# Performance work log

Hardware: AMD Instinct MI355X
Metric: run time of the kernel (lower is better)

The kernel has to match this reference:

```python
import jax, jax.numpy as jnp
import numpy as np

N = 20000          # num proposals (nodes)
E = 320000         # num edges
IN = 4096          # roi feature dim
EMB = 200          # glove embed dim
HID = 512          # hidden dim
NH = 8             # heads (conv1)
HC = HID // NH     # 64 per-head channels
NCLS = 151         # VG object classes
NEG_SLOPE = 0.2    # PyG GATConv leaky_relu slope


def setup_inputs() -> dict:
    key = jax.random.key(0)
    ks = jax.random.split(key, 18)
    d_in1 = IN + EMB + 128  # 4424, conv1 input dim
    inp = {
        "roi_features": jax.random.normal(ks[0], (N, IN), jnp.float32),
        "box_info": jax.random.uniform(ks[1], (N, 9), jnp.float32),
        # embedding tables
        "emb1": jax.random.normal(ks[2], (NCLS, EMB), jnp.float32) * 0.02,
        "emb2": jax.random.normal(ks[3], (NCLS, EMB), jnp.float32) * 0.02,
        # bbox MLP 9 -> 32 -> 128
        "bw1": jax.random.normal(ks[4], (9, 32), jnp.float32) / np.sqrt(9),
        "bb1": jnp.zeros((32,), jnp.float32),
        "bw2": jax.random.normal(ks[5], (32, 128), jnp.float32) / np.sqrt(32),
        "bb2": jnp.zeros((128,), jnp.float32),
        # GATConv1: d_in1 -> 8 heads x 64, concat
        "W1": jax.random.normal(ks[6], (d_in1, NH * HC), jnp.float32) / np.sqrt(d_in1),
        "a_src1": jax.random.normal(ks[7], (NH, HC), jnp.float32) * 0.1,
        "a_dst1": jax.random.normal(ks[8], (NH, HC), jnp.float32) * 0.1,
        "bias1": jnp.zeros((NH * HC,), jnp.float32),
        # GATConv2: 512 -> 512, 1 head, concat=False
        "W2": jax.random.normal(ks[9], (HID, HID), jnp.float32) / np.sqrt(HID),
        "a_src2": jax.random.normal(ks[10], (1, HID), jnp.float32) * 0.1,
        "a_dst2": jax.random.normal(ks[11], (1, HID), jnp.float32) * 0.1,
        "bias2": jnp.zeros((HID,), jnp.float32),
        # int inputs
        "obj_labels": jax.random.randint(ks[12], (N,), 0, NCLS, jnp.int32),
        "edge_index": jax.random.randint(ks[13], (2, E), 0, N, jnp.int32),
    }
    return inp


def _segment_softmax(logits, seg, n):
    # logits: [E, H]; softmax over edges sharing the same destination seg id
    m = jax.ops.segment_max(logits, seg, num_segments=n)
    e = jnp.exp(logits - m[seg])
    s = jax.ops.segment_sum(e, seg, num_segments=n)
    return e / (s[seg] + 1e-16)


def _gat_conv(x, src, dst, W, a_src, a_dst, bias, concat):
    # PyG GATConv (self-loops already included in src/dst); dropout off (eval)
    n = x.shape[0]
    H, C = a_src.shape
    h = (x @ W).reshape(n, H, C)                      # [N, H, C]
    al_s = jnp.einsum('nhc,hc->nh', h, a_src)         # [N, H]
    al_d = jnp.einsum('nhc,hc->nh', h, a_dst)
    logits = jax.nn.leaky_relu(al_s[src] + al_d[dst], NEG_SLOPE)  # [E, H]
    alpha = _segment_softmax(logits, dst, n)          # [E, H]
    out = jax.ops.segment_sum(alpha[:, :, None] * h[src], dst, num_segments=n)
    out = out.reshape(n, H * C) if concat else out.mean(axis=1)
    return out + bias


def reference(roi_features, box_info, emb1, emb2, bw1, bb1, bw2, bb2,
              W1, a_src1, a_dst1, bias1, W2, a_src2, a_dst2, bias2,
              obj_labels, edge_index):
    n = roi_features.shape[0]
    # predcls mode: GT labels -> embedding lookup
    obj_embed = emb1[obj_labels]                              # [N, 200]
    pos = jax.nn.relu(box_info @ bw1 + bb1)
    pos = jax.nn.relu(pos @ bw2 + bb2)                        # [N, 128]
    x = jnp.concatenate([roi_features, obj_embed, pos], -1)  # [N, 4424]

    # add self-loops (PyG GATConv default)
    ar = jnp.arange(n, dtype=edge_index.dtype)
    src = jnp.concatenate([edge_index[0], ar])
    dst = jnp.concatenate([edge_index[1], ar])

    edge_f1 = jax.nn.elu(_gat_conv(x, src, dst, W1, a_src1, a_dst1, bias1, True))
    obj_feats = _gat_conv(edge_f1, src, dst, W2, a_src2, a_dst2, bias2, False)

    obj_dists = jax.nn.one_hot(obj_labels, NCLS, dtype=jnp.float32)
    edge_pre_rep = jnp.concatenate([roi_features, obj_feats, emb2[obj_labels]], -1)
    return obj_dists, obj_labels, edge_pre_rep
```

## Files before the change

kernel.cpp:

```cpp
#include <hip/hip_runtime.h>
#include <hip/hip_bf16.h>

#define NNODES 20000
#define NEDGES 320000
#define ETOT   (NEDGES + NNODES)
#define KPAD1  4448
#define MPAD   20096
#define NCLS   151
#define EPRW   4808
#define OUT_LAB_OFF  3020000L
#define OUT_EPR_OFF  3040000L
#define NSLOPE 0.2f

typedef __attribute__((ext_vector_type(8))) short bf16x8;
typedef __attribute__((ext_vector_type(4))) float f32x4;

__device__ __forceinline__ short f2bf(float v) {
  union { __hip_bfloat16 b; short s; } u;
  u.b = __float2bfloat16(v);
  return u.s;
}

__device__ __forceinline__ float bf2f(short s) {
  union { float f; unsigned u; } x;
  x.u = ((unsigned)(unsigned short)s) << 16;
  return x.f;
}

__device__ __forceinline__ void gld16(const short* g, short* l) {
  __builtin_amdgcn_global_load_lds(
      (const __attribute__((address_space(1))) unsigned int*)g,
      (__attribute__((address_space(3))) unsigned int*)l, 16, 0, 0);
}

__global__ __launch_bounds__(256) void build_x_kernel(
    const float* __restrict__ roi, const float* __restrict__ box,
    const float* __restrict__ emb1, const float* __restrict__ emb2,
    const float* __restrict__ bw1, const float* __restrict__ bb1,
    const float* __restrict__ bw2, const float* __restrict__ bb2,
    const int* __restrict__ labels,
    short* __restrict__ x, float* __restrict__ dout) {
  const int n = blockIdx.x;
  const int tid = threadIdx.x;
  __shared__ float hid[32];
  __shared__ float bx[9];
  if (tid < 9) bx[tid] = box[n * 9 + tid];
  __syncthreads();
  if (tid < 32) {
    float a = bb1[tid];
#pragma unroll
    for (int i = 0; i < 9; ++i) a += bx[i] * bw1[i * 32 + tid];
    hid[tid] = a > 0.f ? a : 0.f;
  }
  __syncthreads();
  const long xrow = (long)n * KPAD1;
  if (tid < 128) {
    float a = bb2[tid];
#pragma unroll
    for (int i = 0; i < 32; ++i) a += hid[i] * bw2[i * 128 + tid];
    a = a > 0.f ? a : 0.f;
    x[xrow + 4296 + tid] = f2bf(a);
  }
  if (tid >= 128 && tid < 152) x[xrow + 4424 + (tid - 128)] = 0;
  const int lab = labels[n];
  float* epr = dout + OUT_EPR_OFF + (long)n * EPRW;
#pragma unroll
  for (int j = tid * 4; j < 4096; j += 1024) {
    const float4 v = *(const float4*)&roi[(long)n * 4096 + j];
    *(float4*)&epr[j] = v;
    short4 b;
    b.x = f2bf(v.x); b.y = f2bf(v.y); b.z = f2bf(v.z); b.w = f2bf(v.w);
    *(short4*)&x[xrow + j] = b;
  }
  if (tid < 50) {
    const int j = tid * 4;
    const float4 e1 = *(const float4*)&emb1[lab * 200 + j];
    short4 b;
    b.x = f2bf(e1.x); b.y = f2bf(e1.y); b.z = f2bf(e1.z); b.w = f2bf(e1.w);
    *(short4*)&x[xrow + 4096 + j] = b;
    *(float4*)&epr[4608 + j] = *(const float4*)&emb2[lab * 200 + j];
  }
  for (int j = tid; j < NCLS; j += 256)
    dout[(long)n * NCLS + j] = (j == lab) ? 1.f : 0.f;
  if (tid == 0) dout[OUT_LAB_OFF + n] = (float)lab;
}

__global__ void misc_init_kernel(short* __restrict__ x, short* __restrict__ ef1,
                                 int* __restrict__ deg,
                                 float* __restrict__ als1, float* __restrict__ ald1,
                                 float* __restrict__ als2, float* __restrict__ ald2) {
  const int t = blockIdx.x * 256 + threadIdx.x;
  if (t < 96 * KPAD1) x[(long)NNODES * KPAD1 + t] = 0;
  if (t < 96 * 512)   ef1[(long)NNODES * 512 + t] = 0;
  if (t < NNODES)     deg[t] = 0;
  if (t < MPAD * 8)   { als1[t] = 0.f; ald1[t] = 0.f; }
  if (t < MPAD)       { als2[t] = 0.f; ald2[t] = 0.f; }
}

__global__ __launch_bounds__(256) void transpose_w_kernel(
    const float* __restrict__ W, short* __restrict__ WT, int K, int Kpad, int Ncols) {
  __shared__ float tile[32][33];
  const int n0 = blockIdx.x * 32;
  const int k0 = blockIdx.y * 32;
  const int tx = threadIdx.x;
  const int ty = threadIdx.y;
#pragma unroll
  for (int i = ty; i < 32; i += 8) {
    const int k = k0 + i;
    tile[i][tx] = (k < K) ? W[(long)k * Ncols + (n0 + tx)] : 0.f;
  }
  __syncthreads();
#pragma unroll
  for (int i = ty; i < 32; i += 8) {
    WT[(long)(n0 + i) * Kpad + (k0 + tx)] = f2bf(tile[tx][i]);
  }
}

__global__ __launch_bounds__(256) void gemm_bt(const short* __restrict__ A,
                                               const short* __restrict__ BT,
                                               short* __restrict__ C,
                                               const float* __restrict__ aS,
                                               const float* __restrict__ aD,
                                               float* __restrict__ als,
                                               float* __restrict__ ald,
                                               int Kpad, int Ncols, int H) {
  __shared__ short As[4096];
  __shared__ short Bs[4096];
  const int tid = threadIdx.x;
  const int lane = tid & 63;
  const int w = tid >> 6;
  const int wr = w >> 1, wc = w & 1;
  const long bm = (long)blockIdx.x * 128;
  const long bn = (long)blockIdx.y * 128;

  f32x4 acc[4][4] = {};

  const short* gA0 = A + (bm + w * 32 + (lane >> 2)) * (long)Kpad + (lane & 3) * 8;
  const short* gA1 = gA0 + 16L * Kpad;
  const short* gB0 = BT + (bn + w * 32 + (lane >> 2)) * (long)Kpad + (lane & 3) * 8;
  const short* gB1 = gB0 + 16L * Kpad;
  short* lA0 = &As[w * 1024];
  short* lA1 = &As[w * 1024 + 512];
  short* lB0 = &Bs[w * 1024];
  short* lB1 = &Bs[w * 1024 + 512];

  const int ar = (wr * 64 + (lane & 15)) * 32 + (lane >> 4) * 8;
  const int br = (wc * 64 + (lane & 15)) * 32 + (lane >> 4) * 8;

  for (int k0 = 0; k0 < Kpad; k0 += 32) {
    gld16(gA0, lA0); gld16(gA1, lA1);
    gld16(gB0, lB0); gld16(gB1, lB1);
    gA0 += 32; gA1 += 32; gB0 += 32; gB1 += 32;
    asm volatile("s_waitcnt vmcnt(0)" ::: "memory");
    __syncthreads();
    bf16x8 a[4], b[4];
#pragma unroll
    for (int mi = 0; mi < 4; ++mi) a[mi] = *(const bf16x8*)&As[ar + mi * 512];
#pragma unroll
    for (int ni = 0; ni < 4; ++ni) b[ni] = *(const bf16x8*)&Bs[br + ni * 512];
#pragma unroll
    for (int mi = 0; mi < 4; ++mi)
#pragma unroll
      for (int ni = 0; ni < 4; ++ni)
        acc[mi][ni] = __builtin_amdgcn_mfma_f32_16x16x32_bf16(a[mi], b[ni], acc[mi][ni], 0, 0, 0);
    __syncthreads();
  }

#pragma unroll
  for (int mi = 0; mi < 4; ++mi) {
#pragma unroll
    for (int ni = 0; ni < 4; ++ni) {
      const long row0 = bm + wr * 64 + mi * 16 + (lane >> 4) * 4;
      const long col  = bn + wc * 64 + ni * 16 + (lane & 15);
#pragma unroll
      for (int r = 0; r < 4; ++r)
        C[(row0 + r) * (long)Ncols + col] = f2bf(acc[mi][ni][r]);
    }
  }

  const int colb = (int)bn + wc * 64 + (lane & 15);
  float asv[4], adv[4];
#pragma unroll
  for (int ni = 0; ni < 4; ++ni) {
    asv[ni] = aS[colb + ni * 16];
    adv[ni] = aD[colb + ni * 16];
  }
  const int head = (H == 8) ? (((int)bn >> 6) + wc) : 0;
#pragma unroll
  for (int mi = 0; mi < 4; ++mi) {
#pragma unroll
    for (int r = 0; r < 4; ++r) {
      float s = 0.f, d = 0.f;
#pragma unroll
      for (int ni = 0; ni < 4; ++ni) {
        const float v = acc[mi][ni][r];
        s += v * asv[ni];
        d += v * adv[ni];
      }
#pragma unroll
      for (int o = 1; o < 16; o <<= 1) {
        s += __shfl_xor(s, o);
        d += __shfl_xor(d, o);
      }
      if ((lane & 15) == 0) {
        const long row = bm + wr * 64 + mi * 16 + (lane >> 4) * 4 + r;
        atomicAdd(&als[row * H + head], s);
        atomicAdd(&ald[row * H + head], d);
      }
    }
  }
}

__global__ void deg_count_kernel(const int* __restrict__ ei, int* __restrict__ deg) {
  const int e = blockIdx.x * 256 + threadIdx.x;
  if (e >= ETOT) return;
  const int d = (e < NEDGES) ? ei[NEDGES + e] : (e - NEDGES);
  atomicAdd(&deg[d], 1);
}

__global__ __launch_bounds__(256) void scan_kernel(const int* __restrict__ deg,
                                                   int* __restrict__ off,
                                                   int* __restrict__ cur) {
  __shared__ int part[256];
  const int tid = threadIdx.x;
  const int chunk = (NNODES + 255) / 256;
  int start = tid * chunk;
  int end = start + chunk; if (end > NNODES) end = NNODES;
  int s = 0;
  for (int i = start; i < end; ++i) s += deg[i];
  part[tid] = s;
  __syncthreads();
  for (int d = 1; d < 256; d <<= 1) {
    const int v = (tid >= d) ? part[tid - d] : 0;
    __syncthreads();
    part[tid] += v;
    __syncthreads();
  }
  int base = part[tid] - s;
  for (int i = start; i < end; ++i) { off[i] = base; cur[i] = base; base += deg[i]; }
}

__global__ void csr_fill_kernel(const int* __restrict__ ei, int* __restrict__ cur,
                                int* __restrict__ csrs) {
  const int e = blockIdx.x * 256 + threadIdx.x;
  if (e >= ETOT) return;
  const int s = (e < NEDGES) ? ei[e] : (e - NEDGES);
  const int d = (e < NEDGES) ? ei[NEDGES + e] : (e - NEDGES);
  csrs[atomicAdd(&cur[d], 1)] = s;
}

__global__ __launch_bounds__(256) void gather1_kernel(const int* __restrict__ off,
    const int* __restrict__ csrs,
    const float* __restrict__ als, const float* __restrict__ ald,
    const short* __restrict__ h1, const float* __restrict__ bias,
    short* __restrict__ ef1) {
  const int dn = blockIdx.x * 4 + (threadIdx.x >> 6);
  const int lane = threadIdx.x & 63;
  const int c0 = lane * 8;
  const int head = lane >> 3;
  const int beg = off[dn];
  const int end = (dn == NNODES - 1) ? ETOT : off[dn + 1];
  const float ad = ald[dn * 8 + head];
  float sum = 0.f;
  float acc[8] = {};
  for (int i = beg; i < end; ++i) {
    const int s = csrs[i];
    float l = als[s * 8 + head] + ad;
    l = l > 0.f ? l : NSLOPE * l;
    const float wgt = expf(l);
    sum += wgt;
    const bf16x8 hv = *(const bf16x8*)&h1[(long)s * 512 + c0];
#pragma unroll
    for (int j = 0; j < 8; ++j) acc[j] += wgt * bf2f(hv[j]);
  }
  const float inv = 1.f / (sum + 1e-16f);
  bf16x8 outv;
#pragma unroll
  for (int j = 0; j < 8; ++j) {
    float r = acc[j] * inv + bias[c0 + j];
    r = r > 0.f ? r : expm1f(r);
    outv[j] = f2bf(r);
  }
  *(bf16x8*)&ef1[(long)dn * 512 + c0] = outv;
}

__global__ __launch_bounds__(256) void gather2_kernel(const int* __restrict__ off,
    const int* __restrict__ csrs,
    const float* __restrict__ als, const float* __restrict__ ald,
    const short* __restrict__ h2, const float* __restrict__ bias,
    float* __restrict__ dout) {
  const int dn = blockIdx.x * 4 + (threadIdx.x >> 6);
  const int lane = threadIdx.x & 63;
  const int c0 = lane * 8;
  const int beg = off[dn];
  const int end = (dn == NNODES - 1) ? ETOT : off[dn + 1];
  const float ad = ald[dn];
  float sum = 0.f;
  float acc[8] = {};
  for (int i = beg; i < end; ++i) {
    const int s = csrs[i];
    float l = als[s] + ad;
    l = l > 0.f ? l : NSLOPE * l;
    const float wgt = expf(l);
    sum += wgt;
    const bf16x8 hv = *(const bf16x8*)&h2[(long)s * 512 + c0];
#pragma unroll
    for (int j = 0; j < 8; ++j) acc[j] += wgt * bf2f(hv[j]);
  }
  const float inv = 1.f / (sum + 1e-16f);
  float* epr = dout + OUT_EPR_OFF + (long)dn * EPRW + 4096;
  float4 o0, o1;
  o0.x = acc[0] * inv + bias[c0 + 0];
  o0.y = acc[1] * inv + bias[c0 + 1];
  o0.z = acc[2] * inv + bias[c0 + 2];
  o0.w = acc[3] * inv + bias[c0 + 3];
  o1.x = acc[4] * inv + bias[c0 + 4];
  o1.y = acc[5] * inv + bias[c0 + 5];
  o1.z = acc[6] * inv + bias[c0 + 6];
  o1.w = acc[7] * inv + bias[c0 + 7];
  *(float4*)&epr[c0]     = o0;
  *(float4*)&epr[c0 + 4] = o1;
}

extern "C" void kernel_launch(void* const* d_in, const int* in_sizes, int n_in,
                              void* d_out, int out_size, void* d_ws, size_t ws_size,
                              hipStream_t stream) {
  const float* roi  = (const float*)d_in[0];
  const float* box  = (const float*)d_in[1];
  const float* emb1 = (const float*)d_in[2];
  const float* emb2 = (const float*)d_in[3];
  const float* bw1  = (const float*)d_in[4];
  const float* bb1  = (const float*)d_in[5];
  const float* bw2  = (const float*)d_in[6];
  const float* bb2  = (const float*)d_in[7];
  const float* W1   = (const float*)d_in[8];
  const float* as1  = (const float*)d_in[9];
  const float* ad1  = (const float*)d_in[10];
  const float* b1   = (const float*)d_in[11];
  const float* W2   = (const float*)d_in[12];
  const float* as2  = (const float*)d_in[13];
  const float* ad2  = (const float*)d_in[14];
  const float* b2   = (const float*)d_in[15];
  const int* labels = (const int*)d_in[16];
  const int* ei     = (const int*)d_in[17];
  float* dout = (float*)d_out;

  char* wsb = (char*)d_ws;
  size_t o = 0;
  auto alloc = [&](size_t bytes) -> void* {
    void* p = wsb + o;
    o += (bytes + 255) & ~(size_t)255;
    return p;
  };
  short* x    = (short*)alloc((size_t)MPAD * KPAD1 * 2);
  short* w1t  = (short*)alloc((size_t)512 * KPAD1 * 2);
  short* h1   = (short*)alloc((size_t)MPAD * 512 * 2);
  short* ef1  = (short*)alloc((size_t)MPAD * 512 * 2);
  short* w2t  = (short*)alloc((size_t)512 * 512 * 2);
  short* h2   = (short*)alloc((size_t)MPAD * 512 * 2);
  float* als1 = (float*)alloc((size_t)MPAD * 8 * 4);
  float* ald1 = (float*)alloc((size_t)MPAD * 8 * 4);
  float* als2 = (float*)alloc((size_t)MPAD * 4);
  float* ald2 = (float*)alloc((size_t)MPAD * 4);
  int*   deg  = (int*)alloc((size_t)NNODES * 4);
  int*   offs = (int*)alloc((size_t)NNODES * 4);
  int*   cur  = (int*)alloc((size_t)NNODES * 4);
  int*   csrs = (int*)alloc((size_t)ETOT * 4);

  const int EB = (ETOT + 255) / 256;

  hipLaunchKernelGGL(build_x_kernel, dim3(NNODES), dim3(256), 0, stream,
                     roi, box, emb1, emb2, bw1, bb1, bw2, bb2, labels, x, dout);
  hipLaunchKernelGGL(misc_init_kernel, dim3((96 * KPAD1 + 255) / 256), dim3(256), 0, stream,
                     x, ef1, deg, als1, ald1, als2, ald2);
  hipLaunchKernelGGL(transpose_w_kernel, dim3(512 / 32, KPAD1 / 32), dim3(32, 8), 0, stream,
                     W1, w1t, 4424, KPAD1, 512);
  hipLaunchKernelGGL(transpose_w_kernel, dim3(512 / 32, 512 / 32), dim3(32, 8), 0, stream,
                     W2, w2t, 512, 512, 512);
  hipLaunchKernelGGL(deg_count_kernel, dim3(EB), dim3(256), 0, stream, ei, deg);
  hipLaunchKernelGGL(scan_kernel, dim3(1), dim3(256), 0, stream, deg, offs, cur);
  hipLaunchKernelGGL(csr_fill_kernel, dim3(EB), dim3(256), 0, stream, ei, cur, csrs);
  hipLaunchKernelGGL(gemm_bt, dim3(MPAD / 128, 4), dim3(256), 0, stream,
                     x, w1t, h1, as1, ad1, als1, ald1, KPAD1, 512, 8);
  hipLaunchKernelGGL(gather1_kernel, dim3(NNODES / 4), dim3(256), 0, stream,
                     offs, csrs, als1, ald1, h1, b1, ef1);
  hipLaunchKernelGGL(gemm_bt, dim3(MPAD / 128, 4), dim3(256), 0, stream,
                     ef1, w2t, h2, as2, ad2, als2, ald2, 512, 512, 1);
  hipLaunchKernelGGL(gather2_kernel, dim3(NNODES / 4), dim3(256), 0, stream,
                     offs, csrs, als2, ald2, h2, b2, dout);
}
```

Measured before the change: 593.0 us.

## Precompute class-embedding projection, shrink GEMM K, merge prep kernels and overlap CSR fill

Removes the 200-wide embedding columns from the conv1 GEMM by precomputing emb1 @ W1 per class (151x512 table) and adding the looked-up row in the GEMM epilogue, cutting K from 4448 to 4224. It merges the build, init, weight-transpose, degree-count and table kernels into one multi-role launch, and folds CSR fill into extra blocks of the first GEMM launch so it runs alongside it. It also uses nontemporal stores for large output writes and adds bounds clamps on CSR slots. The trade-off is epilogue gathers from the E1 table plus branch-heavy mixed-role blocks.

```diff
diff --git a/kernel.cpp b/kernel.cpp
--- a/kernel.cpp
+++ b/kernel.cpp
@@ -4,7 +4,7 @@
 #define NNODES 20000
 #define NEDGES 320000
 #define ETOT   (NEDGES + NNODES)
-#define KPAD1  4448
+#define KPADX  4224
 #define MPAD   20096
 #define NCLS   151
 #define EPRW   4808
@@ -14,6 +14,7 @@
 
 typedef __attribute__((ext_vector_type(8))) short bf16x8;
 typedef __attribute__((ext_vector_type(4))) float f32x4;
+typedef __attribute__((ext_vector_type(4))) short s16x4;
 
 __device__ __forceinline__ short f2bf(float v) {
   union { __hip_bfloat16 b; short s; } u;
@@ -33,189 +34,119 @@
       (__attribute__((address_space(3))) unsigned int*)l, 16, 0, 0);
 }
 
-__global__ __launch_bounds__(256) void build_x_kernel(
+#define PB0 20000
+#define PB1 (PB0 + 1584)
+#define PB2 (PB1 + 2112)
+#define PB3 (PB2 + 256)
+#define PB4 (PB3 + 1329)
+#define PB5 (PB4 + 151)
+
+__global__ __launch_bounds__(256) void mega_prep_kernel(
     const float* __restrict__ roi, const float* __restrict__ box,
     const float* __restrict__ emb1, const float* __restrict__ emb2,
     const float* __restrict__ bw1, const float* __restrict__ bb1,
     const float* __restrict__ bw2, const float* __restrict__ bb2,
-    const int* __restrict__ labels,
-    short* __restrict__ x, float* __restrict__ dout) {
-  const int n = blockIdx.x;
+    const float* __restrict__ W1, const float* __restrict__ W2,
+    const int* __restrict__ labels, const int* __restrict__ ei,
+    short* __restrict__ x, short* __restrict__ w1t, short* __restrict__ w2t,
+    short* __restrict__ ef1, int* __restrict__ deg,
+    float* __restrict__ als1, float* __restrict__ ald1,
+    float* __restrict__ als2, float* __restrict__ ald2,
+    float* __restrict__ E1, float* __restrict__ dout) {
+  const int b = blockIdx.x;
   const int tid = threadIdx.x;
+
   __shared__ float hid[32];
   __shared__ float bx[9];
-  if (tid < 9) bx[tid] = box[n * 9 + tid];
-  __syncthreads();
-  if (tid < 32) {
-    float a = bb1[tid];
-#pragma unroll
-    for (int i = 0; i < 9; ++i) a += bx[i] * bw1[i * 32 + tid];
-    hid[tid] = a > 0.f ? a : 0.f;
-  }
-  __syncthreads();
-  const long xrow = (long)n * KPAD1;
-  if (tid < 128) {
-    float a = bb2[tid];
-#pragma unroll
-    for (int i = 0; i < 32; ++i) a += hid[i] * bw2[i * 128 + tid];
-    a = a > 0.f ? a : 0.f;
-    x[xrow + 4296 + tid] = f2bf(a);
-  }
-  if (tid >= 128 && tid < 152) x[xrow + 4424 + (tid - 128)] = 0;
-  const int lab = labels[n];
-  float* epr = dout + OUT_EPR_OFF + (long)n * EPRW;
-#pragma unroll
-  for (int j = tid * 4; j < 4096; j += 1024) {
-    const float4 v = *(const float4*)&roi[(long)n * 4096 + j];
-    *(float4*)&epr[j] = v;
-    short4 b;
-    b.x = f2bf(v.x); b.y = f2bf(v.y); b.z = f2bf(v.z); b.w = f2bf(v.w);
-    *(short4*)&x[xrow + j] = b;
-  }
-  if (tid < 50) {
-    const int j = tid * 4;
-    const float4 e1 = *(const float4*)&emb1[lab * 200 + j];
-    short4 b;
-    b.x = f2bf(e1.x); b.y = f2bf(e1.y); b.z = f2bf(e1.z); b.w = f2bf(e1.w);
-    *(short4*)&x[xrow + 4096 + j] = b;
-    *(float4*)&epr[4608 + j] = *(const float4*)&emb2[lab * 200 + j];
-  }
-  for (int j = tid; j < NCLS; j += 256)
-    dout[(long)n * NCLS + j] = (j == lab) ? 1.f : 0.f;
-  if (tid == 0) dout[OUT_LAB_OFF + n] = (float)lab;
-}
-
-__global__ void misc_init_kernel(short* __restrict__ x, short* __restrict__ ef1,
-                                 int* __restrict__ deg,
-                                 float* __restrict__ als1, float* __restrict__ ald1,
-                                 float* __restrict__ als2, float* __restrict__ ald2) {
-  const int t = blockIdx.x * 256 + threadIdx.x;
-  if (t < 96 * KPAD1) x[(long)NNODES * KPAD1 + t] = 0;
-  if (t < 96 * 512)   ef1[(long)NNODES * 512 + t] = 0;
-  if (t < NNODES)     deg[t] = 0;
-  if (t < MPAD * 8)   { als1[t] = 0.f; ald1[t] = 0.f; }
-  if (t < MPAD)       { als2[t] = 0.f; ald2[t] = 0.f; }
-}
-
-__global__ __launch_bounds__(256) void transpose_w_kernel(
-    const float* __restrict__ W, short* __restrict__ WT, int K, int Kpad, int Ncols) {
   __shared__ float tile[32][33];
-  const int n0 = blockIdx.x * 32;
-  const int k0 = blockIdx.y * 32;
-  const int tx = threadIdx.x;
-  const int ty = threadIdx.y;
-#pragma unroll
-  for (int i = ty; i < 32; i += 8) {
-    const int k = k0 + i;
-    tile[i][tx] = (k < K) ? W[(long)k * Ncols + (n0 + tx)] : 0.f;
-  }
-  __syncthreads();
-#pragma unroll
-  for (int i = ty; i < 32; i += 8) {
-    WT[(long)(n0 + i) * Kpad + (k0 + tx)] = f2bf(tile[tx][i]);
-  }
-}
-
-__global__ __launch_bounds__(256) void gemm_bt(const short* __restrict__ A,
-                                               const short* __restrict__ BT,
-                                               short* __restrict__ C,
-                                               const float* __restrict__ aS,
-                                               const float* __restrict__ aD,
-                                               float* __restrict__ als,
-                                               float* __restrict__ ald,
-                                               int Kpad, int Ncols, int H) {
-  __shared__ short As[4096];
-  __shared__ short Bs[4096];
-  const int tid = threadIdx.x;
-  const int lane = tid & 63;
-  const int w = tid >> 6;
-  const int wr = w >> 1, wc = w & 1;
-  const long bm = (long)blockIdx.x * 128;
-  const long bn = (long)blockIdx.y * 128;
-
-  f32x4 acc[4][4] = {};
-
-  const short* gA0 = A + (bm + w * 32 + (lane >> 2)) * (long)Kpad + (lane & 3) * 8;
-  const short* gA1 = gA0 + 16L * Kpad;
-  const short* gB0 = BT + (bn + w * 32 + (lane >> 2)) * (long)Kpad + (lane & 3) * 8;
-  const short* gB1 = gB0 + 16L * Kpad;
-  short* lA0 = &As[w * 1024];
-  short* lA1 = &As[w * 1024 + 512];
-  short* lB0 = &Bs[w * 1024];
-  short* lB1 = &Bs[w * 1024 + 512];
-
-  const int ar = (wr * 64 + (lane & 15)) * 32 + (lane >> 4) * 8;
-  const int br = (wc * 64 + (lane & 15)) * 32 + (lane >> 4) * 8;
-
-  for (int k0 = 0; k0 < Kpad; k0 += 32) {
-    gld16(gA0, lA0); gld16(gA1, lA1);
-    gld16(gB0, lB0); gld16(gB1, lB1);
-    gA0 += 32; gA1 += 32; gB0 += 32; gB1 += 32;
-    asm volatile("s_waitcnt vmcnt(0)" ::: "memory");
-    __syncthreads();
-    bf16x8 a[4], b[4];
-#pragma unroll
-    for (int mi = 0; mi < 4; ++mi) a[mi] = *(const bf16x8*)&As[ar + mi * 512];
-#pragma unroll
-    for (int ni = 0; ni < 4; ++ni) b[ni] = *(const bf16x8*)&Bs[br + ni * 512];
-#pragma unroll
-    for (int mi = 0; mi < 4; ++mi)
-#pragma unroll
-      for (int ni = 0; ni < 4; ++ni)
-        acc[mi][ni] = __builtin_amdgcn_mfma_f32_16x16x32_bf16(a[mi], b[ni], acc[mi][ni], 0, 0, 0);
-    __syncthreads();
-  }
-
-#pragma unroll
-  for (int mi = 0; mi < 4; ++mi) {
-#pragma unroll
-    for (int ni = 0; ni < 4; ++ni) {
-      const long row0 = bm + wr * 64 + mi * 16 + (lane >> 4) * 4;
-      const long col  = bn + wc * 64 + ni * 16 + (lane & 15);
-#pragma unroll
-      for (int r = 0; r < 4; ++r)
-        C[(row0 + r) * (long)Ncols + col] = f2bf(acc[mi][ni][r]);
-    }
-  }
-
-  const int colb = (int)bn + wc * 64 + (lane & 15);
-  float asv[4], adv[4];
-#pragma unroll
-  for (int ni = 0; ni < 4; ++ni) {
-    asv[ni] = aS[colb + ni * 16];
-    adv[ni] = aD[colb + ni * 16];
-  }
-  const int head = (H == 8) ? (((int)bn >> 6) + wc) : 0;
-#pragma unroll
-  for (int mi = 0; mi < 4; ++mi) {
-#pragma unroll
-    for (int r = 0; r < 4; ++r) {
-      float s = 0.f, d = 0.f;
-#pragma unroll
-      for (int ni = 0; ni < 4; ++ni) {
-        const float v = acc[mi][ni][r];
-        s += v * asv[ni];
-        d += v * adv[ni];
-      }
-#pragma unroll
-      for (int o = 1; o < 16; o <<= 1) {
-        s += __shfl_xor(s, o);
-        d += __shfl_xor(d, o);
-      }
-      if ((lane & 15) == 0) {
-        const long row = bm + wr * 64 + mi * 16 + (lane >> 4) * 4 + r;
-        atomicAdd(&als[row * H + head], s);
-        atomicAdd(&ald[row * H + head], d);
-      }
-    }
-  }
-}
-
-__global__ void deg_count_kernel(const int* __restrict__ ei, int* __restrict__ deg) {
-  const int e = blockIdx.x * 256 + threadIdx.x;
-  if (e >= ETOT) return;
-  const int d = (e < NEDGES) ? ei[NEDGES + e] : (e - NEDGES);
-  atomicAdd(&deg[d], 1);
+
+  if (b < PB0) {
+    const int n = b;
+    if (tid < 9) bx[tid] = box[n * 9 + tid];
+    __syncthreads();
+    if (tid < 32) {
+      float a = bb1[tid];
+#pragma unroll
+      for (int i = 0; i < 9; ++i) a += bx[i] * bw1[i * 32 + tid];
+      hid[tid] = a > 0.f ? a : 0.f;
+    }
+    __syncthreads();
+    const long xrow = (long)n * KPADX;
+    if (tid < 128) {
+      float a = bb2[tid];
+#pragma unroll
+      for (int i = 0; i < 32; ++i) a += hid[i] * bw2[i * 128 + tid];
+      a = a > 0.f ? a : 0.f;
+      x[xrow + 4096 + tid] = f2bf(a);
+    }
+    const int lab = labels[n];
+    float* epr = dout + OUT_EPR_OFF + (long)n * EPRW;
+#pragma unroll
+    for (int j = tid * 4; j < 4096; j += 1024) {
+      const f32x4 v = *(const f32x4*)&roi[(long)n * 4096 + j];
+      __builtin_nontemporal_store(v, (f32x4*)&epr[j]);
+      s16x4 bb;
+      bb.x = f2bf(v.x); bb.y = f2bf(v.y); bb.z = f2bf(v.z); bb.w = f2bf(v.w);
+      __builtin_nontemporal_store(bb, (s16x4*)&x[xrow + j]);
+    }
+    if (tid < 50) {
+      const int j = tid * 4;
+      const f32x4 e2 = *(const f32x4*)&emb2[lab * 200 + j];
+      __builtin_nontemporal_store(e2, (f32x4*)&epr[4608 + j]);
+    }
+    for (int j = tid; j < NCLS; j += 256)
+      dout[(long)n * NCLS + j] = (j == lab) ? 1.f : 0.f;
+    if (tid == 0) dout[OUT_LAB_OFF + n] = (float)lab;
+  } else if (b < PB1) {
+    const int t = (b - PB0) * 256 + tid;
+    if (t < 96 * KPADX) x[(long)NNODES * KPADX + t] = 0;
+    if (t < 96 * 512)   ef1[(long)NNODES * 512 + t] = 0;
+    if (t < MPAD * 8)   { als1[t] = 0.f; ald1[t] = 0.f; }
+    if (t < MPAD)       { als2[t] = 0.f; ald2[t] = 0.f; }
+  } else if (b < PB2) {
+    const int t = b - PB1;
+    const int n0 = (t % 16) * 32;
+    const int k0 = (t / 16) * 32;
+    const int tx = tid & 31, ty = tid >> 5;
+#pragma unroll
+    for (int i = ty; i < 32; i += 8) {
+      const int kp = k0 + i;
+      const int src = kp < 4096 ? kp : kp + 200;
+      tile[i][tx] = W1[(long)src * 512 + (n0 + tx)];
+    }
+    __syncthreads();
+#pragma unroll
+    for (int i = ty; i < 32; i += 8)
+      w1t[(long)(n0 + i) * KPADX + (k0 + tx)] = f2bf(tile[tx][i]);
+  } else if (b < PB3) {
+    const int t = b - PB2;
+    const int n0 = (t % 16) * 32;
+    const int k0 = (t / 16) * 32;
+    const int tx = tid & 31, ty = tid >> 5;
+#pragma unroll
+    for (int i = ty; i < 32; i += 8)
+      tile[i][tx] = W2[(long)(k0 + i) * 512 + (n0 + tx)];
+    __syncthreads();
+#pragma unroll
+    for (int i = ty; i < 32; i += 8)
+      w2t[(long)(n0 + i) * 512 + (k0 + tx)] = f2bf(tile[tx][i]);
+  } else if (b < PB4) {
+    const int e = (b - PB3) * 256 + tid;
+    if (e < ETOT) {
+      const int d = (e < NEDGES) ? ei[NEDGES + e] : (e - NEDGES);
+      atomicAdd(&deg[d], 1);
+    }
+  } else {
+    const int c = b - PB4;
+#pragma unroll
+    for (int jj = 0; jj < 2; ++jj) {
+      const int j = tid + jj * 256;
+      float a = 0.f;
+      for (int k = 0; k < 200; ++k)
+        a += emb1[c * 200 + k] * W1[(long)(4096 + k) * 512 + j];
+      E1[c * 512 + j] = a;
+    }
+  }
 }
 
 __global__ __launch_bounds__(256) void scan_kernel(const int* __restrict__ deg,
@@ -240,13 +171,135 @@
   for (int i = start; i < end; ++i) { off[i] = base; cur[i] = base; base += deg[i]; }
 }
 
-__global__ void csr_fill_kernel(const int* __restrict__ ei, int* __restrict__ cur,
-                                int* __restrict__ csrs) {
-  const int e = blockIdx.x * 256 + threadIdx.x;
-  if (e >= ETOT) return;
-  const int s = (e < NEDGES) ? ei[e] : (e - NEDGES);
-  const int d = (e < NEDGES) ? ei[NEDGES + e] : (e - NEDGES);
-  csrs[atomicAdd(&cur[d], 1)] = s;
+__global__ __launch_bounds__(256) void gemm_bt(const short* __restrict__ A,
+                                               const short* __restrict__ BT,
+                                               short* __restrict__ C,
+                                               const float* __restrict__ aS,
+                                               const float* __restrict__ aD,
+                                               float* __restrict__ als,
+                                               float* __restrict__ ald,
+                                               const float* __restrict__ E1,
+                                               const int* __restrict__ labels,
+                                               const int* __restrict__ ei,
+                                               int* __restrict__ cur,
+                                               int* __restrict__ csrs,
+                                               int Kpad, int Ncols, int H,
+                                               int nbx) {
+  const int tid = threadIdx.x;
+  const int ngemm = nbx * (Ncols >> 7);
+  if ((int)blockIdx.x >= ngemm) {
+    if (ei) {
+      const int e = ((int)blockIdx.x - ngemm) * 256 + tid;
+      if (e < ETOT) {
+        const int s = (e < NEDGES) ? ei[e] : (e - NEDGES);
+        const int d = (e < NEDGES) ? ei[NEDGES + e] : (e - NEDGES);
+        unsigned slot = (unsigned)atomicAdd(&cur[d], 1);
+        if (slot >= ETOT) slot = 0;
+        csrs[slot] = s;
+      }
+    }
+    return;
+  }
+  __shared__ short As[4096];
+  __shared__ short Bs[4096];
+  const int lane = tid & 63;
+  const int w = tid >> 6;
+  const int wr = w >> 1, wc = w & 1;
+  const long bm = (long)((int)blockIdx.x % nbx) * 128;
+  const long bn = (long)((int)blockIdx.x / nbx) * 128;
+
+  f32x4 acc[4][4] = {};
+
+  const short* gA0 = A + (bm + w * 32 + (lane >> 2)) * (long)Kpad + (lane & 3) * 8;
+  const short* gA1 = gA0 + 16L * Kpad;
+  const short* gB0 = BT + (bn + w * 32 + (lane >> 2)) * (long)Kpad + (lane & 3) * 8;
+  const short* gB1 = gB0 + 16L * Kpad;
+  short* lA0 = &As[w * 1024];
+  short* lA1 = &As[w * 1024 + 512];
+  short* lB0 = &Bs[w * 1024];
+  short* lB1 = &Bs[w * 1024 + 512];
+
+  const int ar = (wr * 64 + (lane & 15)) * 32 + (lane >> 4) * 8;
+  const int br = (wc * 64 + (lane & 15)) * 32 + (lane >> 4) * 8;
+
+  for (int k0 = 0; k0 < Kpad; k0 += 32) {
+    gld16(gA0, lA0); gld16(gA1, lA1);
+    gld16(gB0, lB0); gld16(gB1, lB1);
+    gA0 += 32; gA1 += 32; gB0 += 32; gB1 += 32;
+    asm volatile("s_waitcnt vmcnt(0)" ::: "memory");
+    __syncthreads();
+    bf16x8 a[4], b[4];
+#pragma unroll
+    for (int mi = 0; mi < 4; ++mi) a[mi] = *(const bf16x8*)&As[ar + mi * 512];
+#pragma unroll
+    for (int ni = 0; ni < 4; ++ni) b[ni] = *(const bf16x8*)&Bs[br + ni * 512];
+#pragma unroll
+    for (int mi = 0; mi < 4; ++mi)
+#pragma unroll
+      for (int ni = 0; ni < 4; ++ni)
+        acc[mi][ni] = __builtin_amdgcn_mfma_f32_16x16x32_bf16(a[mi], b[ni], acc[mi][ni], 0, 0, 0);
+    __syncthreads();
+  }
+
+  const int colb = (int)bn + wc * 64 + (lane & 15);
+
+  if (E1) {
+#pragma unroll
+    for (int mi = 0; mi < 4; ++mi) {
+#pragma unroll
+      for (int r = 0; r < 4; ++r) {
+        const long row = bm + wr * 64 + mi * 16 + (lane >> 4) * 4 + r;
+        const int lb = (row < NNODES) ? labels[row] : 0;
+        const float* e1r = E1 + (long)lb * 512;
+#pragma unroll
+        for (int ni = 0; ni < 4; ++ni)
+          acc[mi][ni][r] += e1r[colb + ni * 16];
+      }
+    }
+  }
+
+#pragma unroll
+  for (int mi = 0; mi < 4; ++mi) {
+#pragma unroll
+    for (int ni = 0; ni < 4; ++ni) {
+      const long row0 = bm + wr * 64 + mi * 16 + (lane >> 4) * 4;
+      const long col  = bn + wc * 64 + ni * 16 + (lane & 15);
+#pragma unroll
+      for (int r = 0; r < 4; ++r)
+        C[(row0 + r) * (long)Ncols + col] = f2bf(acc[mi][ni][r]);
+    }
+  }
+
+  float asv[4], adv[4];
+#pragma unroll
+  for (int ni = 0; ni < 4; ++ni) {
+    asv[ni] = aS[colb + ni * 16];
+    adv[ni] = aD[colb + ni * 16];
+  }
+  const int head = (H == 8) ? (((int)bn >> 6) + wc) : 0;
+#pragma unroll
+  for (int mi = 0; mi < 4; ++mi) {
+#pragma unroll
+    for (int r = 0; r < 4; ++r) {
+      float s = 0.f, d = 0.f;
+#pragma unroll
+      for (int ni = 0; ni < 4; ++ni) {
+        const float v = acc[mi][ni][r];
+        s += v * asv[ni];
+        d += v * adv[ni];
+      }
+#pragma unroll
+      for (int o = 1; o < 16; o <<= 1) {
+        s += __shfl_xor(s, o);
+        d += __shfl_xor(d, o);
+      }
+      if ((lane & 15) == 0) {
+        const long row = bm + wr * 64 + mi * 16 + (lane >> 4) * 4 + r;
+        atomicAdd(&als[row * H + head], s);
+        atomicAdd(&ald[row * H + head], d);
+      }
+    }
+  }
 }
 
 __global__ __launch_bounds__(256) void gather1_kernel(const int* __restrict__ off,
@@ -264,7 +317,8 @@
   float sum = 0.f;
   float acc[8] = {};
   for (int i = beg; i < end; ++i) {
-    const int s = csrs[i];
+    int s = csrs[i];
+    if ((unsigned)s >= NNODES) s = 0;
     float l = als[s * 8 + head] + ad;
     l = l > 0.f ? l : NSLOPE * l;
     const float wgt = expf(l);
@@ -298,7 +352,8 @@
   float sum = 0.f;
   float acc[8] = {};
   for (int i = beg; i < end; ++i) {
-    const int s = csrs[i];
+    int s = csrs[i];
+    if ((unsigned)s >= NNODES) s = 0;
     float l = als[s] + ad;
     l = l > 0.f ? l : NSLOPE * l;
     const float wgt = expf(l);
@@ -309,7 +364,7 @@
   }
   const float inv = 1.f / (sum + 1e-16f);
   float* epr = dout + OUT_EPR_OFF + (long)dn * EPRW + 4096;
-  float4 o0, o1;
+  f32x4 o0, o1;
   o0.x = acc[0] * inv + bias[c0 + 0];
   o0.y = acc[1] * inv + bias[c0 + 1];
   o0.z = acc[2] * inv + bias[c0 + 2];
@@ -318,8 +373,8 @@
   o1.y = acc[5] * inv + bias[c0 + 5];
   o1.z = acc[6] * inv + bias[c0 + 6];
   o1.w = acc[7] * inv + bias[c0 + 7];
-  *(float4*)&epr[c0]     = o0;
-  *(float4*)&epr[c0 + 4] = o1;
+  __builtin_nontemporal_store(o0, (f32x4*)&epr[c0]);
+  __builtin_nontemporal_store(o1, (f32x4*)&epr[c0 + 4]);
 }
 
 extern "C" void kernel_launch(void* const* d_in, const int* in_sizes, int n_in,
@@ -352,8 +407,8 @@
     o += (bytes + 255) & ~(size_t)255;
     return p;
   };
-  short* x    = (short*)alloc((size_t)MPAD * KPAD1 * 2);
-  short* w1t  = (short*)alloc((size_t)512 * KPAD1 * 2);
+  short* x    = (short*)alloc((size_t)MPAD * KPADX * 2);
+  short* w1t  = (short*)alloc((size_t)512 * KPADX * 2);
   short* h1   = (short*)alloc((size_t)MPAD * 512 * 2);
   short* ef1  = (short*)alloc((size_t)MPAD * 512 * 2);
   short* w2t  = (short*)alloc((size_t)512 * 512 * 2);
@@ -362,6 +417,7 @@
   float* ald1 = (float*)alloc((size_t)MPAD * 8 * 4);
   float* als2 = (float*)alloc((size_t)MPAD * 4);
   float* ald2 = (float*)alloc((size_t)MPAD * 4);
+  float* E1   = (float*)alloc((size_t)NCLS * 512 * 4);
   int*   deg  = (int*)alloc((size_t)NNODES * 4);
   int*   offs = (int*)alloc((size_t)NNODES * 4);
   int*   cur  = (int*)alloc((size_t)NNODES * 4);
@@ -369,23 +425,23 @@
 
   const int EB = (ETOT + 255) / 256;
 
-  hipLaunchKernelGGL(build_x_kernel, dim3(NNODES), dim3(256), 0, stream,
-                     roi, box, emb1, emb2, bw1, bb1, bw2, bb2, labels, x, dout);
-  hipLaunchKernelGGL(misc_init_kernel, dim3((96 * KPAD1 + 255) / 256), dim3(256), 0, stream,
-                     x, ef1, deg, als1, ald1, als2, ald2);
-  hipLaunchKernelGGL(transpose_w_kernel, dim3(512 / 32, KPAD1 / 32), dim3(32, 8), 0, stream,
-                     W1, w1t, 4424, KPAD1, 512);
-  hipLaunchKernelGGL(transpose_w_kernel, dim3(512 / 32, 512 / 32), dim3(32, 8), 0, stream,
-                     W2, w2t, 512, 512, 512);
-  hipLaunchKernelGGL(deg_count_kernel, dim3(EB), dim3(256), 0, stream, ei, deg);
+  hipMemsetAsync(deg, 0, (size_t)NNODES * 4, stream);
+
+  hipLaunchKernelGGL(mega_prep_kernel, dim3(PB5), dim3(256), 0, stream,
+                     roi, box, emb1, emb2, bw1, bb1, bw2, bb2, W1, W2,
+                     labels, ei, x, w1t, w2t, ef1, deg,
+                     als1, ald1, als2, ald2, E1, dout);
   hipLaunchKernelGGL(scan_kernel, dim3(1), dim3(256), 0, stream, deg, offs, cur);
-  hipLaunchKernelGGL(csr_fill_kernel, dim3(EB), dim3(256), 0, stream, ei, cur, csrs);
-  hipLaunchKernelGGL(gemm_bt, dim3(MPAD / 128, 4), dim3(256), 0, stream,
-                     x, w1t, h1, as1, ad1, als1, ald1, KPAD1, 512, 8);
+  hipLaunchKernelGGL(gemm_bt, dim3(157 * 4 + EB), dim3(256), 0, stream,
+                     x, w1t, h1, as1, ad1, als1, ald1, E1, labels,
+                     ei, cur, csrs, KPADX, 512, 8, 157);
   hipLaunchKernelGGL(gather1_kernel, dim3(NNODES / 4), dim3(256), 0, stream,
                      offs, csrs, als1, ald1, h1, b1, ef1);
-  hipLaunchKernelGGL(gemm_bt, dim3(MPAD / 128, 4), dim3(256), 0, stream,
-                     ef1, w2t, h2, as2, ad2, als2, ald2, 512, 512, 1);
+  hipLaunchKernelGGL(gemm_bt, dim3(157 * 4), dim3(256), 0, stream,
+                     ef1, w2t, h2, as2, ad2, als2, ald2,
+                     (const float*)nullptr, (const int*)nullptr,
+                     (const int*)nullptr, (int*)nullptr, (int*)nullptr,
+                     512, 512, 1, 157);
   hipLaunchKernelGGL(gather2_kernel, dim3(NNODES / 4), dim3(256), 0, stream,
                      offs, csrs, als2, ald2, h2, b2, dout);
 }
```

After: 646.1 us. +9.0%, slower.
